# Performance work log

Hardware: AMD Instinct MI355X
Metric: run time of the kernel (lower is better)

## Reference

```python
import jax, jax.numpy as jnp
import numpy as np


def setup_inputs() -> dict:
    key = jax.random.key(0)
    k1, k2, k3, k4 = jax.random.split(key, 4)
    B, N, F, H, O = 4, 2048, 256, 8, 256
    nodes = jax.random.normal(k1, (B, N, F), dtype=jnp.float32)
    W_heads = jax.random.normal(k2, (H, F, F), dtype=jnp.float32) * (1.0 / np.sqrt(F))
    W_out = jax.random.normal(k3, (H * F, O), dtype=jnp.float32) * (1.0 / np.sqrt(H * F))
    bias = jax.random.normal(k4, (O,), dtype=jnp.float32) * 0.02
    return {"nodes": nodes, "W_heads": W_heads, "W_out": W_out, "bias": bias}


def reference(nodes, W_heads, W_out, bias):
    # nodes: [B,N,F]; W_heads: [H,F,F]; W_out: [H*F,O]; bias: [O]
    B, N, F = nodes.shape
    H = W_heads.shape[0]
    norm = 1.0 / jnp.sqrt(jnp.asarray(F, dtype=nodes.dtype))
    # per-head bilinear scores: (x @ W_h) @ x^T  -> [B,H,N,N]
    xw = jnp.einsum('bnf,hfg->bhng', nodes, W_heads)
    scores = jnp.einsum('bhng,bmg->bhnm', xw, nodes) * norm
    att = jax.nn.softmax(scores, axis=-1)
    # messages: att @ x (V = input nodes) -> [B,H,N,F]
    msgs = jnp.einsum('bhnm,bmf->bhnf', att, nodes)
    # concat heads along feature axis (head 0 first) -> [B,N,H*F]
    msgs = msgs.transpose(0, 2, 1, 3).reshape(B, N, H * F)
    return jnp.matmul(msgs, W_out) + bias
```

## Files before the change

kernel.cpp:

```cpp
#include <hip/hip_runtime.h>
#include <hip/hip_bf16.h>

#define B_ 4
#define N_ 2048
#define F_ 256
#define H_ 8
#define O_ 256

#define SCALE_QK 0.09016844005556021f

typedef __attribute__((ext_vector_type(8))) short short8;
typedef __attribute__((ext_vector_type(4))) short s16x4;
typedef __attribute__((ext_vector_type(4))) float f32x4;
typedef __attribute__((ext_vector_type(4))) unsigned int u32x4;

static __device__ __forceinline__ float bf2f(short u) {
    unsigned int x = ((unsigned int)(unsigned short)u) << 16;
    return __builtin_bit_cast(float, x);
}
static __device__ __forceinline__ short f2bf(float f) {
    unsigned int x = __builtin_bit_cast(unsigned int, f);
    unsigned int lsb = (x >> 16) & 1u;
    x += 0x7fffu + lsb;
    return (short)(x >> 16);
}
static __device__ __forceinline__ unsigned int cvtpk(float a, float b) {
    unsigned int r;
    asm("v_cvt_pk_bf16_f32 %0, %1, %2" : "=v"(r) : "v"(a), "v"(b));
    return r;
}

static __device__ __forceinline__ void gld16(const short* g, short* l) {
    __builtin_amdgcn_global_load_lds(
        (const __attribute__((address_space(1))) void*)g,
        (__attribute__((address_space(3))) void*)l, 16, 0, 0);
}

__global__ __launch_bounds__(256) void cvtT_kernel(const float* __restrict__ src,
                                                   short* __restrict__ dstT,
                                                   short* __restrict__ dst2,
                                                   int R, int C) {
    __shared__ short tile[32][33];
    src  += (size_t)blockIdx.z * R * C;
    dstT += (size_t)blockIdx.z * R * C;
    if (dst2) dst2 += (size_t)blockIdx.z * R * C;
    int tx = threadIdx.x, ty = threadIdx.y;
    int c0 = blockIdx.x * 32, r0 = blockIdx.y * 32;
#pragma unroll
    for (int j = 0; j < 4; j++) {
        int r = r0 + ty + j * 8;
        short v = f2bf(src[(size_t)r * C + c0 + tx]);
        tile[ty + j * 8][tx] = v;
        if (dst2) dst2[(size_t)r * C + c0 + tx] = v;
    }
    __syncthreads();
#pragma unroll
    for (int j = 0; j < 4; j++) {
        int c = c0 + ty + j * 8;
        dstT[(size_t)c * R + r0 + tx] = tile[tx][ty + j * 8];
    }
}

__global__ __launch_bounds__(256) void cvt_kernel(const float* __restrict__ src,
                                                  short* __restrict__ dst, int n) {
    int i = blockIdx.x * 256 + threadIdx.x;
    if (i < n) dst[i] = f2bf(src[i]);
}

template <int NCT>
__device__ __forceinline__ void gemm64_bt(const short* __restrict__ A, int lda,
                                          const short* __restrict__ Bt, int ldb,
                                          float* __restrict__ C, int ldc,
                                          int K, const short* __restrict__ bias) {
    __shared__ short sA[64][72];
    __shared__ short sB[NCT * 16][72];
    int tid = threadIdx.x;
    int w = tid >> 6, l = tid & 63, lq = l & 15, quad = l >> 4;
    f32x4 acc[NCT];
#pragma unroll
    for (int i = 0; i < NCT; i++) acc[i] = (f32x4)(0.f);

    for (int kb = 0; kb < K; kb += 64) {
        __syncthreads();
#pragma unroll
        for (int i = 0; i < 2; i++) {
            int idx = tid + i * 256; int r = idx >> 3, c = (idx & 7) * 8;
            *(short8*)&sA[r][c] = *(const short8*)&A[(size_t)r * lda + kb + c];
        }
#pragma unroll
        for (int i = 0; i < NCT / 2; i++) {
            int idx = tid + i * 256; int r = idx >> 3, c = (idx & 7) * 8;
            *(short8*)&sB[r][c] = *(const short8*)&Bt[(size_t)r * ldb + kb + c];
        }
        __syncthreads();
#pragma unroll
        for (int kk = 0; kk < 2; kk++) {
            short8 af = *(const short8*)&sA[w * 16 + lq][kk * 32 + quad * 8];
#pragma unroll
            for (int ct = 0; ct < NCT; ct++) {
                short8 bf = *(const short8*)&sB[ct * 16 + lq][kk * 32 + quad * 8];
                acc[ct] = __builtin_amdgcn_mfma_f32_16x16x32_bf16(af, bf, acc[ct], 0, 0, 0);
            }
        }
    }
#pragma unroll
    for (int ct = 0; ct < NCT; ct++) {
        int col = ct * 16 + lq;
        float bv = bias ? bf2f(bias[col]) : 0.f;
#pragma unroll
        for (int r = 0; r < 4; r++) {
            int row = w * 16 + quad * 4 + r;
            C[(size_t)row * ldc + col] = acc[ct][r] + bv;
        }
    }
}

__global__ __launch_bounds__(256) void out_kernel(const short* __restrict__ msgs,
                                                  const short* __restrict__ WoutT,
                                                  const short* __restrict__ bias,
                                                  float* __restrict__ out) {
    int mt = blockIdx.x, nt = blockIdx.y;
    gemm64_bt<4>(msgs + (size_t)mt * 64 * (H_ * F_), H_ * F_,
                 WoutT + (size_t)nt * 64 * (H_ * F_), H_ * F_,
                 out + (size_t)mt * 64 * O_ + nt * 64, O_,
                 H_ * F_, bias + nt * 64);
}


#define STAGE_KV(KT, KVF, KVTF) do {                                         \
    _Pragma("unroll")                                                        \
    for (int i_ = 0; i_ < 4; i_++) {                                         \
        int rk_ = w * 8 + i_ * 2 + (l >> 5);                                 \
        int bk_ = (l & 31) ^ (rk_ & 31);                                     \
        gld16(&Xb[(size_t)((KT) * 64 + rk_) * F_ + bk_ * 8],                 \
              &KVF[(w * 8 + i_ * 2) * 256]);                                 \
        int rt_ = w * 32 + i_ * 8 + (l >> 3);                                \
        int bt_ = (l & 7) ^ (rt_ & 7);                                       \
        gld16(&XTb[(size_t)rt_ * N_ + (KT) * 64 + bt_ * 8],                  \
              &KVTF[(w * 32 + i_ * 8) * 64]);                                \
    }                                                                        \
} while (0)

#define COMPUTE_KT(KVF, KVTF) do {                                           \
    f32x4 sacc[4];                                                           \
    _Pragma("unroll")                                                        \
    for (int ct = 0; ct < 4; ct++) sacc[ct] = (f32x4)(0.f);                  \
    __builtin_amdgcn_s_setprio(1);                                           \
    _Pragma("unroll")                                                        \
    for (int kk = 0; kk < 8; kk++) {                                         \
        _Pragma("unroll")                                                    \
        for (int ct = 0; ct < 4; ct++) {                                     \
            int arow = ct * 16 + lq;                                         \
            int ab = (kk * 4 + quad) ^ (arow & 31);                          \
            short8 af = *(const short8*)&KVF[arow * 256 + ab * 8];           \
            sacc[ct] = __builtin_amdgcn_mfma_f32_16x16x32_bf16(af, aq[kk], sacc[ct], 0, 0, 0); \
        }                                                                    \
    }                                                                        \
    __builtin_amdgcn_s_setprio(0);                                           \
    float mx = -INFINITY;                                                    \
    _Pragma("unroll")                                                        \
    for (int ct = 0; ct < 4; ct++)                                           \
        _Pragma("unroll")                                                    \
        for (int r_ = 0; r_ < 4; r_++) mx = fmaxf(mx, sacc[ct][r_]);         \
    mx = fmaxf(mx, __shfl_xor(mx, 16));                                      \
    mx = fmaxf(mx, __shfl_xor(mx, 32));                                      \
    if (!__all(mx - m_q <= 8.0f)) {                \
        float mn = fmaxf(m_q, mx);                                           \
        float alpha = exp2f(m_q - mn);                                       \
        m_q = mn;                                                            \
        l_q *= alpha;                                                        \
        _Pragma("unroll")                                                    \
        for (int ct = 0; ct < 16; ct++)                                      \
            _Pragma("unroll")                                                \
            for (int r_ = 0; r_ < 4; r_++) oacc[ct][r_] *= alpha;            \
    }                                                                        \
    float pv[4][4]; float s_ = 0.f;                                          \
    _Pragma("unroll")                                                        \
    for (int ct = 0; ct < 4; ct++)                                           \
        _Pragma("unroll")                                                    \
        for (int r_ = 0; r_ < 4; r_++) {                                     \
            pv[ct][r_] = exp2f(sacc[ct][r_] - m_q);                          \
            s_ += pv[ct][r_];                                                \
        }                                                                    \
    s_ += __shfl_xor(s_, 16);                                                \
    s_ += __shfl_xor(s_, 32);                                                \
    l_q += s_;                                                               \
    unsigned int w2[4][2];                                                   \
    _Pragma("unroll")                                                        \
    for (int ct = 0; ct < 4; ct++) {                                         \
        w2[ct][0] = cvtpk(pv[ct][0], pv[ct][1]);                             \
        w2[ct][1] = cvtpk(pv[ct][2], pv[ct][3]);                             \
    }                                                                        \
    int sl0 = (2 * (quad & 1)) * 16 + lq;                                    \
    int sl1 = sl0 + 16;                                                      \
    bool hi = (quad >> 1) != 0;                                              \
    short8 pfrag[2];                                                         \
    _Pragma("unroll")                                                        \
    for (int kk = 0; kk < 2; kk++) {                                         \
        unsigned int u0 = __shfl((int)w2[2 * kk][0], sl0);                   \
        unsigned int u1 = __shfl((int)w2[2 * kk][1], sl0);                   \
        unsigned int u2 = __shfl((int)w2[2 * kk][0], sl1);                   \
        unsigned int u3 = __shfl((int)w2[2 * kk][1], sl1);                   \
        unsigned int v0 = __shfl((int)w2[2 * kk + 1][0], sl0);               \
        unsigned int v1 = __shfl((int)w2[2 * kk + 1][1], sl0);               \
        unsigned int v2 = __shfl((int)w2[2 * kk + 1][0], sl1);               \
        unsigned int v3 = __shfl((int)w2[2 * kk + 1][1], sl1);               \
        u32x4 pk = { hi ? v0 : u0, hi ? v1 : u1, hi ? v2 : u2, hi ? v3 : u3 }; \
        pfrag[kk] = __builtin_bit_cast(short8, pk);                          \
    }                                                                        \
    __builtin_amdgcn_s_setprio(1);                                           \
    _Pragma("unroll")                                                        \
    for (int ct = 0; ct < 16; ct++) {                                        \
        int arow = ct * 16 + lq;                                             \
        short8 a0 = *(const short8*)&KVTF[arow * 64 + ((quad) ^ (arow & 7)) * 8]; \
        short8 a1 = *(const short8*)&KVTF[arow * 64 + ((4 + quad) ^ (arow & 7)) * 8]; \
        oacc[ct] = __builtin_amdgcn_mfma_f32_16x16x32_bf16(a0, pfrag[0], oacc[ct], 0, 0, 0); \
        oacc[ct] = __builtin_amdgcn_mfma_f32_16x16x32_bf16(a1, pfrag[1], oacc[ct], 0, 0, 0); \
    }                                                                        \
    __builtin_amdgcn_s_setprio(0);                                           \
} while (0)

__global__ __launch_bounds__(512) void attn_kernel(const short* __restrict__ X,
                                                   const short* __restrict__ WhT,
                                                   const short* __restrict__ XT,
                                                   short* __restrict__ msgs) {
    __shared__ short kvfA[64 * 256];
    __shared__ short kvfB[64 * 256];
    __shared__ short kvTfA[256 * 64];
    __shared__ short kvTfB[256 * 64];

    int qt = blockIdx.x, bh = blockIdx.y, b = bh >> 3, h = bh & 7;
    int tid = threadIdx.x, w = tid >> 6, l = tid & 63, lq = l & 15, quad = l >> 4;
    int q0 = qt * 128;

    const short* Xb  = X  + (size_t)b * N_ * F_;
    const short* XTb = XT + (size_t)b * F_ * N_;
    const short* Whh = WhT + (size_t)h * F_ * F_;

    f32x4 oacc[16];
    short8 aq[8];

#pragma unroll
    for (int i = 0; i < 16; i++) oacc[i] = (f32x4)(0.f);
    {
        short* xdst = (w < 4) ? kvfA : kvfB;
        int wl = w & 3;
#pragma unroll
        for (int i = 0; i < 8; i++) {
            int r = wl * 16 + i * 2 + (l >> 5);
            int bb = (l & 31) ^ (r & 31);
            gld16(&Xb[(size_t)(q0 + ((w >> 2) * 64) + r) * F_ + bb * 8],
                  &xdst[(wl * 16 + i * 2) * 256]);
        }
    }
    const short* xsrc = (w < 4) ? kvfA : kvfB;
#pragma unroll 1
    for (int kb = 0; kb < 4; kb++) {
        __syncthreads();
#pragma unroll
        for (int i = 0; i < 4; i++) {
            int rt = w * 32 + i * 8 + (l >> 3);
            int bt = (l & 7) ^ (rt & 7);
            gld16(&Whh[(size_t)rt * F_ + kb * 64 + bt * 8], &kvTfA[(w * 32 + i * 8) * 64]);
        }
        __syncthreads();
#pragma unroll
        for (int kk = 0; kk < 2; kk++) {
            int arow = (w & 3) * 16 + lq;
            int ab = (kb * 8 + kk * 4 + quad) ^ (arow & 31);
            short8 af = *(const short8*)&xsrc[arow * 256 + ab * 8];
#pragma unroll
            for (int ct = 0; ct < 16; ct++) {
                int brow = ct * 16 + lq;
                int bb = (kk * 4 + quad) ^ (brow & 7);
                short8 bf = *(const short8*)&kvTfA[brow * 64 + bb * 8];
                oacc[ct] = __builtin_amdgcn_mfma_f32_16x16x32_bf16(af, bf, oacc[ct], 0, 0, 0);
            }
        }
    }
    __syncthreads();
    {
        short* qdst = (w < 4) ? kvTfA : kvTfB;
#pragma unroll
        for (int ct = 0; ct < 16; ct++) {
#pragma unroll
            for (int r = 0; r < 4; r++) {
                int row = (w & 3) * 16 + quad * 4 + r;
                int col = ct * 16 + lq;
                int pb = (col >> 3) ^ (row & 31);
                qdst[row * 256 + pb * 8 + (col & 7)] = f2bf(oacc[ct][r] * SCALE_QK);
            }
        }
        __syncthreads();
#pragma unroll
        for (int kk = 0; kk < 8; kk++) {
            int row = (w & 3) * 16 + lq;
            int ab = (kk * 4 + quad) ^ (row & 31);
            aq[kk] = *(const short8*)&qdst[row * 256 + ab * 8];
        }
    }
    __syncthreads();

#pragma unroll
    for (int i = 0; i < 16; i++) oacc[i] = (f32x4)(0.f);
    float m_q = -INFINITY, l_q = 0.f;

    STAGE_KV(0, kvfA, kvTfA);
    __syncthreads();

#pragma unroll 1
    for (int kt2 = 0; kt2 < 16; kt2++) {
        STAGE_KV(2 * kt2 + 1, kvfB, kvTfB);
        COMPUTE_KT(kvfA, kvTfA);
        __syncthreads();
        STAGE_KV((2 * kt2 + 2) & 31, kvfA, kvTfA);
        COMPUTE_KT(kvfB, kvTfB);
        __syncthreads();
    }

    float inv = 1.f / l_q;
    short* Mout = msgs + (size_t)(b * N_ + q0 + w * 16 + lq) * (H_ * F_) + h * F_;
#pragma unroll
    for (int ct = 0; ct < 16; ct++) {
        s16x4 v4 = { f2bf(oacc[ct][0] * inv), f2bf(oacc[ct][1] * inv),
                     f2bf(oacc[ct][2] * inv), f2bf(oacc[ct][3] * inv) };
        *(s16x4*)&Mout[ct * 16 + quad * 4] = v4;
    }
}

extern "C" void kernel_launch(void* const* d_in, const int* in_sizes, int n_in,
                              void* d_out, int out_size, void* d_ws, size_t ws_size,
                              hipStream_t stream) {
    const float* nodes = (const float*)d_in[0];
    const float* Wh    = (const float*)d_in[1];
    const float* Wout  = (const float*)d_in[2];
    const float* bias  = (const float*)d_in[3];
    float* out = (float*)d_out;

    char* ws = (char*)d_ws;
    short* msgs   = (short*)(ws);
    short* WhT    = (short*)(ws + 33554432);
    short* WoutT  = (short*)(ws + 34603008);
    short* XT     = (short*)(ws + 35651584);
    short* Xbf    = (short*)(ws + 39845888);
    short* biasbf = (short*)(ws + 44040192);

    dim3 tblk(32, 8, 1);
    hipLaunchKernelGGL(cvtT_kernel, dim3(8, 8, 8),  tblk, 0, stream, Wh,    WhT,   (short*)nullptr, 256,  256);
    hipLaunchKernelGGL(cvtT_kernel, dim3(8, 64, 1), tblk, 0, stream, Wout,  WoutT, (short*)nullptr, 2048, 256);
    hipLaunchKernelGGL(cvtT_kernel, dim3(8, 64, 4), tblk, 0, stream, nodes, XT,    Xbf,             2048, 256);
    hipLaunchKernelGGL(cvt_kernel,  dim3(1),    dim3(256), 0, stream, bias, biasbf, 256);

    hipLaunchKernelGGL(attn_kernel, dim3(16, 32), dim3(512), 0, stream, Xbf, WhT, XT, msgs);
    hipLaunchKernelGGL(out_kernel,  dim3(128, 4), dim3(256), 0, stream, msgs, WoutT, biasbf, out);
}
```

Before: 289.2 us.

## Double-buffer output GEMM with async LDS loads, swizzle, and fp32 bias

Rewrites the output projection GEMM to use 512-thread blocks computing 64x128 tiles. It double-buffers shared memory, filled by direct global-to-LDS loads (gld16) with an XOR swizzle, so the next K-tile's fetch overlaps MFMA on the current one. The bias is read directly in fp32, which removes the separate bias conversion launch. The cost is halving the block count to 256, which may reduce occupancy and load balance.

```diff
diff --git a/kernel.cpp b/kernel.cpp
--- a/kernel.cpp
+++ b/kernel.cpp
@@ -61,69 +61,62 @@
     }
 }
 
-__global__ __launch_bounds__(256) void cvt_kernel(const float* __restrict__ src,
-                                                  short* __restrict__ dst, int n) {
-    int i = blockIdx.x * 256 + threadIdx.x;
-    if (i < n) dst[i] = f2bf(src[i]);
-}
-
-template <int NCT>
-__device__ __forceinline__ void gemm64_bt(const short* __restrict__ A, int lda,
-                                          const short* __restrict__ Bt, int ldb,
-                                          float* __restrict__ C, int ldc,
-                                          int K, const short* __restrict__ bias) {
-    __shared__ short sA[64][72];
-    __shared__ short sB[NCT * 16][72];
-    int tid = threadIdx.x;
-    int w = tid >> 6, l = tid & 63, lq = l & 15, quad = l >> 4;
-    f32x4 acc[NCT];
-#pragma unroll
-    for (int i = 0; i < NCT; i++) acc[i] = (f32x4)(0.f);
-
-    for (int kb = 0; kb < K; kb += 64) {
-        __syncthreads();
-#pragma unroll
-        for (int i = 0; i < 2; i++) {
-            int idx = tid + i * 256; int r = idx >> 3, c = (idx & 7) * 8;
-            *(short8*)&sA[r][c] = *(const short8*)&A[(size_t)r * lda + kb + c];
-        }
-#pragma unroll
-        for (int i = 0; i < NCT / 2; i++) {
-            int idx = tid + i * 256; int r = idx >> 3, c = (idx & 7) * 8;
-            *(short8*)&sB[r][c] = *(const short8*)&Bt[(size_t)r * ldb + kb + c];
-        }
-        __syncthreads();
+__global__ __launch_bounds__(512) void out_kernel(const short* __restrict__ msgs,
+                                                  const short* __restrict__ WoutT,
+                                                  const float* __restrict__ bias,
+                                                  float* __restrict__ out) {
+    __shared__ short sA[2][64 * 64];
+    __shared__ short sB[2][128 * 64];
+    int mt = blockIdx.x, nt = blockIdx.y;
+    int tid = threadIdx.x, w = tid >> 6, l = tid & 63, lq = l & 15, quad = l >> 4;
+    const short* Arow = msgs  + (size_t)(mt * 64)  * (H_ * F_);
+    const short* Brow = WoutT + (size_t)(nt * 128) * (H_ * F_);
+    int xk = (l & 7) ^ (l >> 3);
+
+    f32x4 acc[4];
+#pragma unroll
+    for (int i = 0; i < 4; i++) acc[i] = (f32x4)(0.f);
+
+#define STAGE_OUT(KB, BI) do {                                               \
+        gld16(&Arow[(size_t)(w * 8 + (l >> 3)) * (H_ * F_) + (KB) * 64 + xk * 8], \
+              &sA[BI][w * 8 * 64]);                                          \
+        gld16(&Brow[(size_t)(w * 16 + (l >> 3)) * (H_ * F_) + (KB) * 64 + xk * 8], \
+              &sB[BI][w * 16 * 64]);                                         \
+        gld16(&Brow[(size_t)(w * 16 + 8 + (l >> 3)) * (H_ * F_) + (KB) * 64 + xk * 8], \
+              &sB[BI][(w * 16 + 8) * 64]);                                   \
+    } while (0)
+
+    STAGE_OUT(0, 0);
+    __syncthreads();
+
+#pragma unroll 1
+    for (int kb = 0; kb < 32; kb++) {
+        int cur = kb & 1;
+        if (kb < 31) STAGE_OUT(kb + 1, cur ^ 1);
+        int arow = (w & 3) * 16 + lq;
 #pragma unroll
         for (int kk = 0; kk < 2; kk++) {
-            short8 af = *(const short8*)&sA[w * 16 + lq][kk * 32 + quad * 8];
-#pragma unroll
-            for (int ct = 0; ct < NCT; ct++) {
-                short8 bf = *(const short8*)&sB[ct * 16 + lq][kk * 32 + quad * 8];
+            short8 af = *(const short8*)&sA[cur][arow * 64 + (((kk * 4 + quad) ^ (arow & 7)) * 8)];
+#pragma unroll
+            for (int ct = 0; ct < 4; ct++) {
+                int brow = (w >> 2) * 64 + ct * 16 + lq;
+                short8 bf = *(const short8*)&sB[cur][brow * 64 + (((kk * 4 + quad) ^ (brow & 7)) * 8)];
                 acc[ct] = __builtin_amdgcn_mfma_f32_16x16x32_bf16(af, bf, acc[ct], 0, 0, 0);
             }
         }
-    }
-#pragma unroll
-    for (int ct = 0; ct < NCT; ct++) {
-        int col = ct * 16 + lq;
-        float bv = bias ? bf2f(bias[col]) : 0.f;
+        __syncthreads();
+    }
+
+#pragma unroll
+    for (int ct = 0; ct < 4; ct++) {
+        int gcol = nt * 128 + (w >> 2) * 64 + ct * 16 + lq;
+        float bv = bias[gcol];
 #pragma unroll
         for (int r = 0; r < 4; r++) {
-            int row = w * 16 + quad * 4 + r;
-            C[(size_t)row * ldc + col] = acc[ct][r] + bv;
-        }
-    }
-}
-
-__global__ __launch_bounds__(256) void out_kernel(const short* __restrict__ msgs,
-                                                  const short* __restrict__ WoutT,
-                                                  const short* __restrict__ bias,
-                                                  float* __restrict__ out) {
-    int mt = blockIdx.x, nt = blockIdx.y;
-    gemm64_bt<4>(msgs + (size_t)mt * 64 * (H_ * F_), H_ * F_,
-                 WoutT + (size_t)nt * 64 * (H_ * F_), H_ * F_,
-                 out + (size_t)mt * 64 * O_ + nt * 64, O_,
-                 H_ * F_, bias + nt * 64);
+            int row = mt * 64 + (w & 3) * 16 + quad * 4 + r;
+            out[(size_t)row * O_ + gcol] = acc[ct][r] + bv;
+        }
+    }
 }
 
 
@@ -343,14 +336,12 @@
     short* WoutT  = (short*)(ws + 34603008);
     short* XT     = (short*)(ws + 35651584);
     short* Xbf    = (short*)(ws + 39845888);
-    short* biasbf = (short*)(ws + 44040192);
 
     dim3 tblk(32, 8, 1);
     hipLaunchKernelGGL(cvtT_kernel, dim3(8, 8, 8),  tblk, 0, stream, Wh,    WhT,   (short*)nullptr, 256,  256);
     hipLaunchKernelGGL(cvtT_kernel, dim3(8, 64, 1), tblk, 0, stream, Wout,  WoutT, (short*)nullptr, 2048, 256);
     hipLaunchKernelGGL(cvtT_kernel, dim3(8, 64, 4), tblk, 0, stream, nodes, XT,    Xbf,             2048, 256);
-    hipLaunchKernelGGL(cvt_kernel,  dim3(1),    dim3(256), 0, stream, bias, biasbf, 256);
 
     hipLaunchKernelGGL(attn_kernel, dim3(16, 32), dim3(512), 0, stream, Xbf, WhT, XT, msgs);
-    hipLaunchKernelGGL(out_kernel,  dim3(128, 4), dim3(256), 0, stream, msgs, WoutT, biasbf, out);
-}
+    hipLaunchKernelGGL(out_kernel,  dim3(128, 2), dim3(512), 0, stream, msgs, WoutT, bias, out);
+}
```

After: 289.0 us (median of 5 runs). About the same (-0.1%).
